# Kernel tuning notes

Hardware: AMD Instinct MI355X
Metric: run time of the kernel (lower is better)

Reference implementation:

```python
import jax, jax.numpy as jnp
import numpy as np

H = 128  # hidden_dim
F = 64   # node_feat_dim


def setup_inputs() -> dict:
    key = jax.random.key(0)
    ks = jax.random.split(key, 24)
    N, E, NR, NT = 50000, 400000, 20000, 20000
    inp = {
        "mol_x": jax.random.normal(ks[0], (N, F), jnp.float32),
        "pos": jax.random.normal(ks[1], (N, 3), jnp.float32),
        "reaction_x": jax.random.normal(ks[2], (NR, F), jnp.float32),
        "target_x": jax.random.normal(ks[3], (NT, F), jnp.float32),
        "edge_index": jax.random.randint(ks[4], (2, E), 0, N, jnp.int32),
    }
    def lin(k, fan_in, fan_out):
        s = 1.0 / np.sqrt(fan_in)
        kw, kb = jax.random.split(k)
        W = jax.random.uniform(kw, (fan_in, fan_out), jnp.float32, -s, s)
        b = jax.random.uniform(kb, (fan_out,), jnp.float32, -s, s)
        return W, b
    inp["W_node"], inp["b_node"] = lin(ks[5], F, H)
    inp["W_att1"], inp["b_att1"] = lin(ks[6], 2 * H + 3, H)
    inp["W_att2"], inp["b_att2"] = lin(ks[7], H, 1)
    inp["W_upd"], inp["b_upd"] = lin(ks[8], H, H)
    inp["Wy1"], inp["by1"] = lin(ks[9], H, 64)
    inp["Wy2"], inp["by2"] = lin(ks[10], 64, 1)
    inp["Wa1"], inp["ba1"] = lin(ks[11], H, 64)
    inp["Wa2"], inp["ba2"] = lin(ks[12], 64, 1)
    return inp


def reference(mol_x, pos, reaction_x, target_x, edge_index,
              W_node, b_node, W_att1, b_att1, W_att2, b_att2,
              W_upd, b_upd, Wy1, by1, Wy2, by2, Wa1, ba1, Wa2, ba2):
    N = mol_x.shape[0]
    # node encoder
    h = mol_x @ W_node + b_node                      # [N, H]
    src, dst = edge_index[0], edge_index[1]          # PyG: x_j = source, x_i = target
    x_j = h[src]                                      # [E, H]
    x_i = h[dst]                                      # [E, H]
    dist = pos[dst] - pos[src]                        # [E, 3]
    cat = jnp.concatenate([x_i, x_j, dist], axis=1)   # [E, 2H+3]
    s = jax.nn.relu(cat @ W_att1 + b_att1) @ W_att2 + b_att2  # [E, 1]
    att = jax.nn.softmax(s, axis=0)                   # global softmax over edges (dim=0)
    msg = x_j * att                                   # [E, H]
    aggr = jax.ops.segment_sum(msg, dst, num_segments=N)  # scatter-add -> [N, H]
    mol_feats = aggr @ W_upd + b_upd                  # [N, H]
    # heads on reaction / target graphs
    rh = reaction_x @ W_node + b_node
    th = target_x @ W_node + b_node
    pred_yield = (jax.nn.relu(rh @ Wy1 + by1) @ Wy2 + by2).squeeze(-1)
    pred_activity = (jax.nn.relu(th @ Wa1 + ba1) @ Wa2 + ba2).squeeze(-1)
    return pred_yield, pred_activity, mol_feats
```

## Files before the change

### kernel.cpp

```cpp
#include <hip/hip_runtime.h>
#include <hip/hip_bf16.h>

typedef unsigned short ushort_t;
typedef __attribute__((ext_vector_type(8))) short s16x8;
typedef __attribute__((ext_vector_type(4))) float f32x4;

__device__ inline unsigned short f2bf(float x) {
    unsigned u = __float_as_uint(x);
    return (unsigned short)((u + 0x7FFFu + ((u >> 16) & 1u)) >> 16);
}
__device__ inline float bflo(unsigned u) { return __uint_as_float(u << 16); }
__device__ inline float bfhi(unsigned u) { return __uint_as_float(u & 0xffff0000u); }

__device__ inline void pack_one(const float* __restrict__ W, int K, int N,
                                ushort_t* __restrict__ dst, int g) {
    int KT = K / 32;
    int nt = g / (KT * 64);
    int rem = g % (KT * 64);
    int kt = rem / 64, lane = rem % 64;
    int n = nt * 16 + (lane & 15);
    int kbase = kt * 32 + ((lane >> 4) << 3);
    ushort_t tmp[8];
#pragma unroll
    for (int j = 0; j < 8; ++j) tmp[j] = f2bf(W[(size_t)(kbase + j) * N + n]);
    uint4 pk;
    pk.x = tmp[0] | ((unsigned)tmp[1] << 16);
    pk.y = tmp[2] | ((unsigned)tmp[3] << 16);
    pk.z = tmp[4] | ((unsigned)tmp[5] << 16);
    pk.w = tmp[6] | ((unsigned)tmp[7] << 16);
    *(uint4*)&dst[(size_t)g * 8] = pk;
}

__global__ void convert_w(const float* __restrict__ Wn, const float* __restrict__ W1,
                          const float* __restrict__ Wu, const float* __restrict__ Wy1,
                          const float* __restrict__ Wa1,
                          ushort_t* __restrict__ Wnb, ushort_t* __restrict__ W1tb,
                          ushort_t* __restrict__ W1mb, ushort_t* __restrict__ Wub,
                          ushort_t* __restrict__ Wy1b, ushort_t* __restrict__ Wa1b,
                          int* __restrict__ counts, int N) {
    int t = blockIdx.x * 256 + threadIdx.x;
    if (t < 1024)       pack_one(Wn, 64, 128, Wnb, t);
    else if (t < 3072)  pack_one(W1, 128, 128, W1tb, t - 1024);
    else if (t < 5120)  pack_one(W1 + 128 * 128, 128, 128, W1mb, t - 3072);
    else if (t < 7168)  pack_one(Wu, 128, 128, Wub, t - 5120);
    else if (t < 8192)  pack_one(Wy1, 128, 64, Wy1b, t - 7168);
    else if (t < 9216)  pack_one(Wa1, 128, 64, Wa1b, t - 8192);
    if (t < N) counts[t] = 0;
}

__global__ void encode_pq(const float* __restrict__ x, const ushort_t* __restrict__ Wnb,
                          const float* __restrict__ bn, const ushort_t* __restrict__ W1tb,
                          const ushort_t* __restrict__ W1mb, const float* __restrict__ b1,
                          ushort_t* __restrict__ hb, ushort_t* __restrict__ P,
                          ushort_t* __restrict__ Q, const int* __restrict__ dst,
                          int* __restrict__ counts, int nrows, int E) {
    __shared__ ushort_t ldsH[4 * 16 * 136];
    int t = threadIdx.x;
    for (int e = blockIdx.x * 256 + t; e < E; e += gridDim.x * 256)
        atomicAdd(&counts[dst[e]], 1);
    int w = t >> 6, lane = t & 63;
    int c = lane & 15, q = lane >> 4;
    int r0 = blockIdx.x * 64 + w * 16;
    int rowA = r0 + c; if (rowA >= nrows) rowA = nrows - 1;
    ushort_t* myH = &ldsH[w * 16 * 136];

    s16x8 xa[2];
#pragma unroll
    for (int kt = 0; kt < 2; ++kt) {
        const float* xp = &x[(size_t)rowA * 64 + kt * 32 + q * 8];
        float4 v0 = *(const float4*)xp;
        float4 v1 = *(const float4*)(xp + 4);
        s16x8 a;
        a[0] = (short)f2bf(v0.x); a[1] = (short)f2bf(v0.y);
        a[2] = (short)f2bf(v0.z); a[3] = (short)f2bf(v0.w);
        a[4] = (short)f2bf(v1.x); a[5] = (short)f2bf(v1.y);
        a[6] = (short)f2bf(v1.z); a[7] = (short)f2bf(v1.w);
        xa[kt] = a;
    }
#pragma unroll
    for (int nt = 0; nt < 8; ++nt) {
        f32x4 acc = {0.f, 0.f, 0.f, 0.f};
#pragma unroll
        for (int kt = 0; kt < 2; ++kt) {
            s16x8 b = *(const s16x8*)&Wnb[((nt * 2 + kt) * 64 + lane) * 8];
            acc = __builtin_amdgcn_mfma_f32_16x16x32_bf16(xa[kt], b, acc, 0, 0, 0);
        }
        float bi = bn[nt * 16 + c];
#pragma unroll
        for (int r = 0; r < 4; ++r) {
            int row = r0 + q * 4 + r;
            ushort_t hv = f2bf(acc[r] + bi);
            myH[(q * 4 + r) * 136 + nt * 16 + c] = hv;
            if (row < nrows) hb[(size_t)row * 128 + nt * 16 + c] = hv;
        }
    }
    __syncthreads();
    s16x8 ha[4];
#pragma unroll
    for (int kt = 0; kt < 4; ++kt)
        ha[kt] = *(const s16x8*)&myH[c * 136 + kt * 32 + q * 8];
#pragma unroll
    for (int nt = 0; nt < 8; ++nt) {
        f32x4 pa = {0.f, 0.f, 0.f, 0.f}, qa = pa;
#pragma unroll
        for (int kt = 0; kt < 4; ++kt) {
            s16x8 bp = *(const s16x8*)&W1tb[((nt * 4 + kt) * 64 + lane) * 8];
            s16x8 bq = *(const s16x8*)&W1mb[((nt * 4 + kt) * 64 + lane) * 8];
            pa = __builtin_amdgcn_mfma_f32_16x16x32_bf16(ha[kt], bp, pa, 0, 0, 0);
            qa = __builtin_amdgcn_mfma_f32_16x16x32_bf16(ha[kt], bq, qa, 0, 0, 0);
        }
        float bi = b1[nt * 16 + c];
#pragma unroll
        for (int r = 0; r < 4; ++r) {
            int row = r0 + q * 4 + r;
            if (row < nrows) {
                P[(size_t)row * 128 + nt * 16 + c] = f2bf(pa[r] + bi);
                Q[(size_t)row * 128 + nt * 16 + c] = f2bf(qa[r]);
            }
        }
    }
}

__global__ void scan1(const int* __restrict__ counts, int* __restrict__ offs,
                      int* __restrict__ partials, int N) {
    __shared__ int sm[256];
    int i = blockIdx.x * 256 + threadIdx.x;
    int v = (i < N) ? counts[i] : 0;
    sm[threadIdx.x] = v; __syncthreads();
    for (int off = 1; off < 256; off <<= 1) {
        int add = (threadIdx.x >= off) ? sm[threadIdx.x - off] : 0;
        __syncthreads();
        sm[threadIdx.x] += add;
        __syncthreads();
    }
    if (i < N) offs[i] = sm[threadIdx.x] - v;
    if (threadIdx.x == 255) partials[blockIdx.x] = sm[255];
}

__global__ void scan_add(int* __restrict__ offs, int* __restrict__ cursor,
                         const int* __restrict__ partials, int nb, int N) {
    __shared__ int sm[256];
    int t = threadIdx.x;
    sm[t] = (t < nb && t < blockIdx.x) ? partials[t] : 0;
    __syncthreads();
    for (int off = 128; off > 0; off >>= 1) {
        if (t < off) sm[t] += sm[t + off];
        __syncthreads();
    }
    int basev = sm[0];
    int i = blockIdx.x * 256 + t;
    if (i < N) {
        int v = offs[i] + basev;
        offs[i] = v;
        cursor[i] = v;
    }
}

__global__ void edge_score(const ushort_t* __restrict__ P, const ushort_t* __restrict__ Q,
                           const float* __restrict__ pos, const int* __restrict__ src,
                           const int* __restrict__ dst, const float* __restrict__ W1b,
                           const float* __restrict__ W2, const float* __restrict__ b2,
                           int* __restrict__ cursor, int2* __restrict__ csr,
                           float* __restrict__ redm, float* __restrict__ rede, int E) {
    __shared__ float wsh[512];
    __shared__ float smm[256], sme[256];
    int t = threadIdx.x;
    for (int i = t; i < 384; i += 256) wsh[i] = W1b[i];
    if (t < 128) wsh[384 + t] = W2[t];
    __syncthreads();
    int w = t >> 6, lane = t & 63;
    int g = lane >> 4, c = lane & 15;
    float w0[8], w1[8], w2[8], wv[8];
#pragma unroll
    for (int j = 0; j < 8; ++j) {
        w0[j] = wsh[c * 8 + j];
        w1[j] = wsh[128 + c * 8 + j];
        w2[j] = wsh[256 + c * 8 + j];
        wv[j] = wsh[384 + c * 8 + j];
    }
    float b2v = b2[0];
    int base = blockIdx.x * 64 + w * 16;
    float m = -1e30f, ev = 0.f;
#pragma unroll
    for (int it = 0; it < 4; ++it) {
        int e = base + it * 4 + g;
        bool valid = e < E;
        int ee = valid ? e : (E - 1);
        int sa = src[ee], da = dst[ee];
        uint4 pr = *(const uint4*)&P[(size_t)da * 128 + c * 8];
        uint4 qr = *(const uint4*)&Q[(size_t)sa * 128 + c * 8];
        float d0 = pos[da * 3]     - pos[sa * 3];
        float d1 = pos[da * 3 + 1] - pos[sa * 3 + 1];
        float d2 = pos[da * 3 + 2] - pos[sa * 3 + 2];
        unsigned pw[4] = {pr.x, pr.y, pr.z, pr.w};
        unsigned qw[4] = {qr.x, qr.y, qr.z, qr.w};
        float v = 0.f;
#pragma unroll
        for (int jj = 0; jj < 4; ++jj) {
            float pe = bflo(pw[jj]) + bflo(qw[jj])
                     + d0 * w0[2 * jj] + d1 * w1[2 * jj] + d2 * w2[2 * jj];
            float po = bfhi(pw[jj]) + bfhi(qw[jj])
                     + d0 * w0[2 * jj + 1] + d1 * w1[2 * jj + 1] + d2 * w2[2 * jj + 1];
            v += fmaxf(pe, 0.f) * wv[2 * jj] + fmaxf(po, 0.f) * wv[2 * jj + 1];
        }
#pragma unroll
        for (int off = 1; off < 16; off <<= 1) v += __shfl_xor(v, off, 64);
        if (c == 0 && valid) {
            float sv = v + b2v;
            int p = atomicAdd(&cursor[da], 1);
            csr[p] = make_int2(sa, __float_as_int(sv));
            float nm = fmaxf(m, sv);
            ev = ev * __expf(m - nm) + __expf(sv - nm);
            m = nm;
        }
    }
    smm[t] = m; sme[t] = ev; __syncthreads();
    for (int off = 128; off > 0; off >>= 1) {
        if (t < off) {
            float m1 = smm[t], m2 = smm[t + off];
            float e1 = sme[t], e2 = sme[t + off];
            float M = fmaxf(m1, m2);
            smm[t] = M;
            sme[t] = e1 * __expf(m1 - M) + e2 * __expf(m2 - M);
        }
        __syncthreads();
    }
    if (t == 0) { redm[blockIdx.x] = smm[0]; rede[blockIdx.x] = sme[0]; }
}

__global__ void smax2(const float* __restrict__ redm, const float* __restrict__ rede,
                      float* __restrict__ scal, int nb) {
    __shared__ float smm[256], sme[256];
    int t = threadIdx.x;
    float m = -1e30f, ev = 0.f;
    for (int i = t; i < nb; i += 256) {
        float m2 = redm[i], e2 = rede[i];
        float M = fmaxf(m, m2);
        ev = ev * __expf(m - M) + e2 * __expf(m2 - M);
        m = M;
    }
    smm[t] = m; sme[t] = ev; __syncthreads();
    for (int off = 128; off > 0; off >>= 1) {
        if (t < off) {
            float m1 = smm[t], m2 = smm[t + off];
            float e1 = sme[t], e2 = sme[t + off];
            float M = fmaxf(m1, m2);
            smm[t] = M;
            sme[t] = e1 * __expf(m1 - M) + e2 * __expf(m2 - M);
        }
        __syncthreads();
    }
    if (t == 0) { scal[0] = smm[0]; scal[1] = 1.f / sme[0]; }
}

__global__ void gather_upd(const ushort_t* __restrict__ hb, const int2* __restrict__ csr,
                           const int* __restrict__ offs, const int* __restrict__ deg,
                           const float* __restrict__ scal,
                           const ushort_t* __restrict__ Wub, const float* __restrict__ bu,
                           float* __restrict__ C, int N) {
    __shared__ ushort_t ldsA[16 * 136];
    int t = threadIdx.x;
    int w = t >> 6, lane = t & 63;
    int g = lane >> 4, c = lane & 15;
    int r0 = blockIdx.x * 16;
    float m = scal[0], inv = scal[1];
#pragma unroll
    for (int i = 0; i < 4; ++i) {
        int node = r0 + w * 4 + i;
        float a[8] = {0.f, 0.f, 0.f, 0.f, 0.f, 0.f, 0.f, 0.f};
        if (node < N) {
            int start = offs[node], d = deg[node];
            for (int k = g; k < d; k += 4) {
                int2 v = csr[start + k];
                float att = __expf(__int_as_float(v.y) - m) * inv;
                uint4 hq = *(const uint4*)&hb[(size_t)v.x * 128 + c * 8];
                a[0] += bflo(hq.x) * att; a[1] += bfhi(hq.x) * att;
                a[2] += bflo(hq.y) * att; a[3] += bfhi(hq.y) * att;
                a[4] += bflo(hq.z) * att; a[5] += bfhi(hq.z) * att;
                a[6] += bflo(hq.w) * att; a[7] += bfhi(hq.w) * att;
            }
        }
#pragma unroll
        for (int j = 0; j < 8; ++j) {
            a[j] += __shfl_xor(a[j], 16, 64);
            a[j] += __shfl_xor(a[j], 32, 64);
        }
        if (g == 0) {
            uint4 pk;
            pk.x = f2bf(a[0]) | ((unsigned)f2bf(a[1]) << 16);
            pk.y = f2bf(a[2]) | ((unsigned)f2bf(a[3]) << 16);
            pk.z = f2bf(a[4]) | ((unsigned)f2bf(a[5]) << 16);
            pk.w = f2bf(a[6]) | ((unsigned)f2bf(a[7]) << 16);
            *(uint4*)&ldsA[(w * 4 + i) * 136 + c * 8] = pk;
        }
    }
    __syncthreads();
    int q = lane >> 4;
    int ntA = w, ntB = w + 4;
    f32x4 acc0 = {0.f, 0.f, 0.f, 0.f}, acc1 = acc0;
#pragma unroll
    for (int kt = 0; kt < 4; ++kt) {
        s16x8 av = *(const s16x8*)&ldsA[c * 136 + kt * 32 + q * 8];
        s16x8 b0 = *(const s16x8*)&Wub[((ntA * 4 + kt) * 64 + lane) * 8];
        s16x8 b1 = *(const s16x8*)&Wub[((ntB * 4 + kt) * 64 + lane) * 8];
        acc0 = __builtin_amdgcn_mfma_f32_16x16x32_bf16(av, b0, acc0, 0, 0, 0);
        acc1 = __builtin_amdgcn_mfma_f32_16x16x32_bf16(av, b1, acc1, 0, 0, 0);
    }
    float bi0 = bu[ntA * 16 + c], bi1 = bu[ntB * 16 + c];
#pragma unroll
    for (int r = 0; r < 4; ++r) {
        int row = r0 + q * 4 + r;
        if (row < N) {
            C[(size_t)row * 128 + ntA * 16 + c] = acc0[r] + bi0;
            C[(size_t)row * 128 + ntB * 16 + c] = acc1[r] + bi1;
        }
    }
}

__global__ void head_mfma(const float* __restrict__ rx, const float* __restrict__ tx,
                          const ushort_t* __restrict__ Wnb, const float* __restrict__ bn,
                          const ushort_t* __restrict__ Wy1b, const float* __restrict__ by1,
                          const float* __restrict__ Wy2, const float* __restrict__ by2,
                          const ushort_t* __restrict__ Wa1b, const float* __restrict__ ba1,
                          const float* __restrict__ Wa2, const float* __restrict__ ba2,
                          float* __restrict__ out, int nb1, int NR, int NT) {
    __shared__ ushort_t ldsA[16 * 72];
    __shared__ ushort_t ldsB[16 * 136];
    __shared__ float part[64];
    int blk = blockIdx.x;
    const float* x; const ushort_t* W1b; const float* b1; const float* W2; const float* b2;
    float* o; int r0, nrows;
    if (blk < nb1) { x = rx; W1b = Wy1b; b1 = by1; W2 = Wy2; b2 = by2; o = out; r0 = blk * 16; nrows = NR; }
    else { x = tx; W1b = Wa1b; b1 = ba1; W2 = Wa2; b2 = ba2; o = out + NR; r0 = (blk - nb1) * 16; nrows = NT; }

    int t = threadIdx.x;
    {
        int row = t >> 4, c4 = (t & 15) * 4;
        float4 v = *(const float4*)&x[(size_t)(r0 + row) * 64 + c4];
        uint2 pk;
        pk.x = f2bf(v.x) | ((unsigned)f2bf(v.y) << 16);
        pk.y = f2bf(v.z) | ((unsigned)f2bf(v.w) << 16);
        *(uint2*)&ldsA[row * 72 + c4] = pk;
    }
    __syncthreads();
    int w = t >> 6, lane = t & 63;
    int c = lane & 15, q = lane >> 4;
    {
        int ntA = w, ntB = w + 4;
        f32x4 acc0 = {0.f, 0.f, 0.f, 0.f}, acc1 = acc0;
#pragma unroll
        for (int kt = 0; kt < 2; ++kt) {
            s16x8 a = *(const s16x8*)&ldsA[c * 72 + kt * 32 + q * 8];
            s16x8 b0 = *(const s16x8*)&Wnb[((ntA * 2 + kt) * 64 + lane) * 8];
            s16x8 b1v = *(const s16x8*)&Wnb[((ntB * 2 + kt) * 64 + lane) * 8];
            acc0 = __builtin_amdgcn_mfma_f32_16x16x32_bf16(a, b0, acc0, 0, 0, 0);
            acc1 = __builtin_amdgcn_mfma_f32_16x16x32_bf16(a, b1v, acc1, 0, 0, 0);
        }
        float bi0 = bn[ntA * 16 + c], bi1 = bn[ntB * 16 + c];
#pragma unroll
        for (int r = 0; r < 4; ++r) {
            int row = q * 4 + r;
            ldsB[row * 136 + ntA * 16 + c] = f2bf(acc0[r] + bi0);
            ldsB[row * 136 + ntB * 16 + c] = f2bf(acc1[r] + bi1);
        }
    }
    __syncthreads();
    {
        f32x4 acc = {0.f, 0.f, 0.f, 0.f};
#pragma unroll
        for (int kt = 0; kt < 4; ++kt) {
            s16x8 a = *(const s16x8*)&ldsB[c * 136 + kt * 32 + q * 8];
            s16x8 b0 = *(const s16x8*)&W1b[((w * 4 + kt) * 64 + lane) * 8];
            acc = __builtin_amdgcn_mfma_f32_16x16x32_bf16(a, b0, acc, 0, 0, 0);
        }
        float bi = b1[w * 16 + c], w2v = W2[w * 16 + c];
#pragma unroll
        for (int r = 0; r < 4; ++r) {
            float u = fmaxf(acc[r] + bi, 0.f) * w2v;
#pragma unroll
            for (int mm = 1; mm < 16; mm <<= 1) u += __shfl_xor(u, mm, 64);
            if (c == 0) part[w * 16 + q * 4 + r] = u;
        }
    }
    __syncthreads();
    if (t < 16) {
        int row = r0 + t;
        if (row < nrows)
            o[row] = part[t] + part[16 + t] + part[32 + t] + part[48 + t] + b2[0];
    }
}

extern "C" void kernel_launch(void* const* d_in, const int* in_sizes, int n_in,
                              void* d_out, int out_size, void* d_ws, size_t ws_size,
                              hipStream_t stream) {
    const float* mol_x      = (const float*)d_in[0];
    const float* pos        = (const float*)d_in[1];
    const float* reaction_x = (const float*)d_in[2];
    const float* target_x   = (const float*)d_in[3];
    const int*   ei         = (const int*)d_in[4];
    const float* W_node = (const float*)d_in[5];
    const float* b_node = (const float*)d_in[6];
    const float* W_att1 = (const float*)d_in[7];
    const float* b_att1 = (const float*)d_in[8];
    const float* W_att2 = (const float*)d_in[9];
    const float* b_att2 = (const float*)d_in[10];
    const float* W_upd  = (const float*)d_in[11];
    const float* b_upd  = (const float*)d_in[12];
    const float* Wy1 = (const float*)d_in[13];
    const float* by1 = (const float*)d_in[14];
    const float* Wy2 = (const float*)d_in[15];
    const float* by2 = (const float*)d_in[16];
    const float* Wa1 = (const float*)d_in[17];
    const float* ba1 = (const float*)d_in[18];
    const float* Wa2 = (const float*)d_in[19];
    const float* ba2 = (const float*)d_in[20];

    int N  = in_sizes[0] / 64;
    int E  = in_sizes[4] / 2;
    int NR = in_sizes[2] / 64;
    int NT = in_sizes[3] / 64;

    float* out = (float*)d_out;

    int nbE = (E + 63) / 64;

    char* wp = (char*)d_ws;
    ushort_t* hb = (ushort_t*)wp;  wp += (size_t)N * 128 * 2;
    ushort_t* Qb = (ushort_t*)wp;  wp += (size_t)N * 128 * 2;
    float* redm  = (float*)wp;     wp += (size_t)nbE * 4;
    float* rede  = (float*)wp;     wp += (size_t)nbE * 4;
    float* scal  = (float*)wp;     wp += 4 * 4;
    int* counts  = (int*)wp;       wp += (size_t)N * 4;
    int* offs    = (int*)wp;       wp += (size_t)N * 4;
    int* cursor  = (int*)wp;       wp += (size_t)N * 4;
    int* partials= (int*)wp;       wp += 256 * 4;
    int2* csr    = (int2*)wp;      wp += (size_t)E * 8;
    ushort_t* Wnb  = (ushort_t*)wp; wp += 8192 * 2;
    ushort_t* W1tb = (ushort_t*)wp; wp += 16384 * 2;
    ushort_t* W1mb = (ushort_t*)wp; wp += 16384 * 2;
    ushort_t* Wub  = (ushort_t*)wp; wp += 16384 * 2;
    ushort_t* Wy1b = (ushort_t*)wp; wp += 8192 * 2;
    ushort_t* Wa1b = (ushort_t*)wp; wp += 8192 * 2;
    ushort_t* Pb = (ushort_t*)(out + NR + NT);
    float* molf  = out + NR + NT;

    const int* srcp = ei;
    const int* dstp = ei + E;
    int nbN = (N + 255) / 256;

    convert_w<<<nbN, 256, 0, stream>>>(W_node, W_att1, W_upd, Wy1, Wa1,
                                       Wnb, W1tb, W1mb, Wub, Wy1b, Wa1b, counts, N);
    encode_pq<<<(N + 63) / 64, 256, 0, stream>>>(mol_x, Wnb, b_node, W1tb, W1mb, b_att1,
                                                 hb, Pb, Qb, dstp, counts, N, E);
    scan1<<<nbN, 256, 0, stream>>>(counts, offs, partials, N);
    scan_add<<<nbN, 256, 0, stream>>>(offs, cursor, partials, nbN, N);
    edge_score<<<nbE, 256, 0, stream>>>(Pb, Qb, pos, srcp, dstp,
                                        W_att1 + 256 * 128, W_att2, b_att2,
                                        cursor, csr, redm, rede, E);
    smax2<<<1, 256, 0, stream>>>(redm, rede, scal, nbE);
    gather_upd<<<(N + 15) / 16, 256, 0, stream>>>(hb, csr, offs, counts, scal,
                                                  Wub, b_upd, molf, N);
    head_mfma<<<(NR + NT) / 16, 256, 0, stream>>>(reaction_x, target_x, Wnb, b_node,
                                                  Wy1b, by1, Wy2, by2, Wa1b, ba1, Wa2, ba2,
                                                  out, NR / 16, NR, NT);
}
```

Measured before the change: 246.9 us.

## Fuse softmax finalize, gather-update and heads into one kernel; widen edge blocks

Removes the single-block smax2 kernel by having every gather block redundantly reduce the per-block max/sum partials, and merges the gather_upd and head_mfma kernels into one launch split by block index. Edge_score now processes 128 edges per block (halving partials) and issues the cursor atomic before the P/Q loads so its latency overlaps. The gather loop is unrolled by two to keep more loads in flight. This cuts two launches and one serial tiny kernel, at the cost of each gather block reading about 3125 partials redundantly.

```diff
diff --git a/kernel.cpp b/kernel.cpp
--- a/kernel.cpp
+++ b/kernel.cpp
@@ -179,14 +179,16 @@
         wv[j] = wsh[384 + c * 8 + j];
     }
     float b2v = b2[0];
-    int base = blockIdx.x * 64 + w * 16;
+    int base = blockIdx.x * 128 + w * 32;
     float m = -1e30f, ev = 0.f;
 #pragma unroll
-    for (int it = 0; it < 4; ++it) {
+    for (int it = 0; it < 8; ++it) {
         int e = base + it * 4 + g;
         bool valid = e < E;
         int ee = valid ? e : (E - 1);
         int sa = src[ee], da = dst[ee];
+        int p = 0;
+        if (c == 0 && valid) p = atomicAdd(&cursor[da], 1);
         uint4 pr = *(const uint4*)&P[(size_t)da * 128 + c * 8];
         uint4 qr = *(const uint4*)&Q[(size_t)sa * 128 + c * 8];
         float d0 = pos[da * 3]     - pos[sa * 3];
@@ -207,7 +209,6 @@
         for (int off = 1; off < 16; off <<= 1) v += __shfl_xor(v, off, 64);
         if (c == 0 && valid) {
             float sv = v + b2v;
-            int p = atomicAdd(&cursor[da], 1);
             csr[p] = make_int2(sa, __float_as_int(sv));
             float nm = fmaxf(m, sv);
             ev = ev * __expf(m - nm) + __expf(sv - nm);
@@ -228,165 +229,177 @@
     if (t == 0) { redm[blockIdx.x] = smm[0]; rede[blockIdx.x] = sme[0]; }
 }
 
-__global__ void smax2(const float* __restrict__ redm, const float* __restrict__ rede,
-                      float* __restrict__ scal, int nb) {
-    __shared__ float smm[256], sme[256];
-    int t = threadIdx.x;
-    float m = -1e30f, ev = 0.f;
-    for (int i = t; i < nb; i += 256) {
-        float m2 = redm[i], e2 = rede[i];
-        float M = fmaxf(m, m2);
-        ev = ev * __expf(m - M) + e2 * __expf(m2 - M);
-        m = M;
-    }
-    smm[t] = m; sme[t] = ev; __syncthreads();
-    for (int off = 128; off > 0; off >>= 1) {
-        if (t < off) {
-            float m1 = smm[t], m2 = smm[t + off];
-            float e1 = sme[t], e2 = sme[t + off];
-            float M = fmaxf(m1, m2);
-            smm[t] = M;
-            sme[t] = e1 * __expf(m1 - M) + e2 * __expf(m2 - M);
-        }
-        __syncthreads();
-    }
-    if (t == 0) { scal[0] = smm[0]; scal[1] = 1.f / sme[0]; }
-}
-
-__global__ void gather_upd(const ushort_t* __restrict__ hb, const int2* __restrict__ csr,
-                           const int* __restrict__ offs, const int* __restrict__ deg,
-                           const float* __restrict__ scal,
-                           const ushort_t* __restrict__ Wub, const float* __restrict__ bu,
-                           float* __restrict__ C, int N) {
-    __shared__ ushort_t ldsA[16 * 136];
+__global__ void gather_head(const ushort_t* __restrict__ hb, const int2* __restrict__ csr,
+                            const int* __restrict__ offs, const int* __restrict__ deg,
+                            const float* __restrict__ redm, const float* __restrict__ rede,
+                            int nbE,
+                            const ushort_t* __restrict__ Wub, const float* __restrict__ bu,
+                            float* __restrict__ molf, int N, int nbG,
+                            const float* __restrict__ rx, const float* __restrict__ tx,
+                            const ushort_t* __restrict__ Wnb, const float* __restrict__ bn,
+                            const ushort_t* __restrict__ Wy1b, const float* __restrict__ by1,
+                            const float* __restrict__ Wy2, const float* __restrict__ by2,
+                            const ushort_t* __restrict__ Wa1b, const float* __restrict__ ba1,
+                            const float* __restrict__ Wa2, const float* __restrict__ ba2,
+                            float* __restrict__ out, int nb1, int NR, int NT) {
     int t = threadIdx.x;
     int w = t >> 6, lane = t & 63;
-    int g = lane >> 4, c = lane & 15;
-    int r0 = blockIdx.x * 16;
-    float m = scal[0], inv = scal[1];
-#pragma unroll
-    for (int i = 0; i < 4; ++i) {
-        int node = r0 + w * 4 + i;
-        float a[8] = {0.f, 0.f, 0.f, 0.f, 0.f, 0.f, 0.f, 0.f};
-        if (node < N) {
-            int start = offs[node], d = deg[node];
-            for (int k = g; k < d; k += 4) {
-                int2 v = csr[start + k];
-                float att = __expf(__int_as_float(v.y) - m) * inv;
-                uint4 hq = *(const uint4*)&hb[(size_t)v.x * 128 + c * 8];
-                a[0] += bflo(hq.x) * att; a[1] += bfhi(hq.x) * att;
-                a[2] += bflo(hq.y) * att; a[3] += bfhi(hq.y) * att;
-                a[4] += bflo(hq.z) * att; a[5] += bfhi(hq.z) * att;
-                a[6] += bflo(hq.w) * att; a[7] += bfhi(hq.w) * att;
-            }
-        }
-#pragma unroll
-        for (int j = 0; j < 8; ++j) {
-            a[j] += __shfl_xor(a[j], 16, 64);
-            a[j] += __shfl_xor(a[j], 32, 64);
-        }
-        if (g == 0) {
-            uint4 pk;
-            pk.x = f2bf(a[0]) | ((unsigned)f2bf(a[1]) << 16);
-            pk.y = f2bf(a[2]) | ((unsigned)f2bf(a[3]) << 16);
-            pk.z = f2bf(a[4]) | ((unsigned)f2bf(a[5]) << 16);
-            pk.w = f2bf(a[6]) | ((unsigned)f2bf(a[7]) << 16);
-            *(uint4*)&ldsA[(w * 4 + i) * 136 + c * 8] = pk;
-        }
-    }
-    __syncthreads();
-    int q = lane >> 4;
-    int ntA = w, ntB = w + 4;
-    f32x4 acc0 = {0.f, 0.f, 0.f, 0.f}, acc1 = acc0;
-#pragma unroll
-    for (int kt = 0; kt < 4; ++kt) {
-        s16x8 av = *(const s16x8*)&ldsA[c * 136 + kt * 32 + q * 8];
-        s16x8 b0 = *(const s16x8*)&Wub[((ntA * 4 + kt) * 64 + lane) * 8];
-        s16x8 b1 = *(const s16x8*)&Wub[((ntB * 4 + kt) * 64 + lane) * 8];
-        acc0 = __builtin_amdgcn_mfma_f32_16x16x32_bf16(av, b0, acc0, 0, 0, 0);
-        acc1 = __builtin_amdgcn_mfma_f32_16x16x32_bf16(av, b1, acc1, 0, 0, 0);
-    }
-    float bi0 = bu[ntA * 16 + c], bi1 = bu[ntB * 16 + c];
-#pragma unroll
-    for (int r = 0; r < 4; ++r) {
-        int row = r0 + q * 4 + r;
-        if (row < N) {
-            C[(size_t)row * 128 + ntA * 16 + c] = acc0[r] + bi0;
-            C[(size_t)row * 128 + ntB * 16 + c] = acc1[r] + bi1;
-        }
-    }
-}
-
-__global__ void head_mfma(const float* __restrict__ rx, const float* __restrict__ tx,
-                          const ushort_t* __restrict__ Wnb, const float* __restrict__ bn,
-                          const ushort_t* __restrict__ Wy1b, const float* __restrict__ by1,
-                          const float* __restrict__ Wy2, const float* __restrict__ by2,
-                          const ushort_t* __restrict__ Wa1b, const float* __restrict__ ba1,
-                          const float* __restrict__ Wa2, const float* __restrict__ ba2,
-                          float* __restrict__ out, int nb1, int NR, int NT) {
-    __shared__ ushort_t ldsA[16 * 72];
-    __shared__ ushort_t ldsB[16 * 136];
-    __shared__ float part[64];
-    int blk = blockIdx.x;
-    const float* x; const ushort_t* W1b; const float* b1; const float* W2; const float* b2;
-    float* o; int r0, nrows;
-    if (blk < nb1) { x = rx; W1b = Wy1b; b1 = by1; W2 = Wy2; b2 = by2; o = out; r0 = blk * 16; nrows = NR; }
-    else { x = tx; W1b = Wa1b; b1 = ba1; W2 = Wa2; b2 = ba2; o = out + NR; r0 = (blk - nb1) * 16; nrows = NT; }
-
-    int t = threadIdx.x;
-    {
-        int row = t >> 4, c4 = (t & 15) * 4;
-        float4 v = *(const float4*)&x[(size_t)(r0 + row) * 64 + c4];
-        uint2 pk;
-        pk.x = f2bf(v.x) | ((unsigned)f2bf(v.y) << 16);
-        pk.y = f2bf(v.z) | ((unsigned)f2bf(v.w) << 16);
-        *(uint2*)&ldsA[row * 72 + c4] = pk;
-    }
-    __syncthreads();
-    int w = t >> 6, lane = t & 63;
     int c = lane & 15, q = lane >> 4;
-    {
+
+    if (blockIdx.x < nbG) {
+        __shared__ ushort_t ldsA[16 * 136];
+        __shared__ float smm[256], sme[256];
+        float m = -1e30f, z = 0.f;
+        for (int i = t; i < nbE; i += 256) {
+            float m2 = redm[i], z2 = rede[i];
+            float M = fmaxf(m, m2);
+            z = z * __expf(m - M) + z2 * __expf(m2 - M);
+            m = M;
+        }
+        smm[t] = m; sme[t] = z; __syncthreads();
+        for (int off = 128; off > 0; off >>= 1) {
+            if (t < off) {
+                float m1 = smm[t], m2 = smm[t + off];
+                float e1 = sme[t], e2 = sme[t + off];
+                float M = fmaxf(m1, m2);
+                smm[t] = M;
+                sme[t] = e1 * __expf(m1 - M) + e2 * __expf(m2 - M);
+            }
+            __syncthreads();
+        }
+        float gm = smm[0], inv = 1.f / sme[0];
+        __syncthreads();
+
+        int g = lane >> 4;
+        int r0 = blockIdx.x * 16;
+#pragma unroll
+        for (int i = 0; i < 4; ++i) {
+            int node = r0 + w * 4 + i;
+            float a[8] = {0.f, 0.f, 0.f, 0.f, 0.f, 0.f, 0.f, 0.f};
+            if (node < N) {
+                int start = offs[node], d = deg[node];
+                int k = g;
+                for (; k + 4 < d; k += 8) {
+                    int2 v0 = csr[start + k];
+                    int2 v1 = csr[start + k + 4];
+                    uint4 h0 = *(const uint4*)&hb[(size_t)v0.x * 128 + c * 8];
+                    uint4 h1 = *(const uint4*)&hb[(size_t)v1.x * 128 + c * 8];
+                    float at0 = __expf(__int_as_float(v0.y) - gm) * inv;
+                    float at1 = __expf(__int_as_float(v1.y) - gm) * inv;
+                    a[0] += bflo(h0.x) * at0; a[1] += bfhi(h0.x) * at0;
+                    a[2] += bflo(h0.y) * at0; a[3] += bfhi(h0.y) * at0;
+                    a[4] += bflo(h0.z) * at0; a[5] += bfhi(h0.z) * at0;
+                    a[6] += bflo(h0.w) * at0; a[7] += bfhi(h0.w) * at0;
+                    a[0] += bflo(h1.x) * at1; a[1] += bfhi(h1.x) * at1;
+                    a[2] += bflo(h1.y) * at1; a[3] += bfhi(h1.y) * at1;
+                    a[4] += bflo(h1.z) * at1; a[5] += bfhi(h1.z) * at1;
+                    a[6] += bflo(h1.w) * at1; a[7] += bfhi(h1.w) * at1;
+                }
+                if (k < d) {
+                    int2 v0 = csr[start + k];
+                    uint4 h0 = *(const uint4*)&hb[(size_t)v0.x * 128 + c * 8];
+                    float at0 = __expf(__int_as_float(v0.y) - gm) * inv;
+                    a[0] += bflo(h0.x) * at0; a[1] += bfhi(h0.x) * at0;
+                    a[2] += bflo(h0.y) * at0; a[3] += bfhi(h0.y) * at0;
+                    a[4] += bflo(h0.z) * at0; a[5] += bfhi(h0.z) * at0;
+                    a[6] += bflo(h0.w) * at0; a[7] += bfhi(h0.w) * at0;
+                }
+            }
+#pragma unroll
+            for (int j = 0; j < 8; ++j) {
+                a[j] += __shfl_xor(a[j], 16, 64);
+                a[j] += __shfl_xor(a[j], 32, 64);
+            }
+            if (g == 0) {
+                uint4 pk;
+                pk.x = f2bf(a[0]) | ((unsigned)f2bf(a[1]) << 16);
+                pk.y = f2bf(a[2]) | ((unsigned)f2bf(a[3]) << 16);
+                pk.z = f2bf(a[4]) | ((unsigned)f2bf(a[5]) << 16);
+                pk.w = f2bf(a[6]) | ((unsigned)f2bf(a[7]) << 16);
+                *(uint4*)&ldsA[(w * 4 + i) * 136 + c * 8] = pk;
+            }
+        }
+        __syncthreads();
         int ntA = w, ntB = w + 4;
         f32x4 acc0 = {0.f, 0.f, 0.f, 0.f}, acc1 = acc0;
 #pragma unroll
-        for (int kt = 0; kt < 2; ++kt) {
-            s16x8 a = *(const s16x8*)&ldsA[c * 72 + kt * 32 + q * 8];
-            s16x8 b0 = *(const s16x8*)&Wnb[((ntA * 2 + kt) * 64 + lane) * 8];
-            s16x8 b1v = *(const s16x8*)&Wnb[((ntB * 2 + kt) * 64 + lane) * 8];
-            acc0 = __builtin_amdgcn_mfma_f32_16x16x32_bf16(a, b0, acc0, 0, 0, 0);
-            acc1 = __builtin_amdgcn_mfma_f32_16x16x32_bf16(a, b1v, acc1, 0, 0, 0);
-        }
-        float bi0 = bn[ntA * 16 + c], bi1 = bn[ntB * 16 + c];
+        for (int kt = 0; kt < 4; ++kt) {
+            s16x8 av = *(const s16x8*)&ldsA[c * 136 + kt * 32 + q * 8];
+            s16x8 b0 = *(const s16x8*)&Wub[((ntA * 4 + kt) * 64 + lane) * 8];
+            s16x8 b1 = *(const s16x8*)&Wub[((ntB * 4 + kt) * 64 + lane) * 8];
+            acc0 = __builtin_amdgcn_mfma_f32_16x16x32_bf16(av, b0, acc0, 0, 0, 0);
+            acc1 = __builtin_amdgcn_mfma_f32_16x16x32_bf16(av, b1, acc1, 0, 0, 0);
+        }
+        float bi0 = bu[ntA * 16 + c], bi1 = bu[ntB * 16 + c];
 #pragma unroll
         for (int r = 0; r < 4; ++r) {
-            int row = q * 4 + r;
-            ldsB[row * 136 + ntA * 16 + c] = f2bf(acc0[r] + bi0);
-            ldsB[row * 136 + ntB * 16 + c] = f2bf(acc1[r] + bi1);
-        }
-    }
-    __syncthreads();
-    {
-        f32x4 acc = {0.f, 0.f, 0.f, 0.f};
-#pragma unroll
-        for (int kt = 0; kt < 4; ++kt) {
-            s16x8 a = *(const s16x8*)&ldsB[c * 136 + kt * 32 + q * 8];
-            s16x8 b0 = *(const s16x8*)&W1b[((w * 4 + kt) * 64 + lane) * 8];
-            acc = __builtin_amdgcn_mfma_f32_16x16x32_bf16(a, b0, acc, 0, 0, 0);
-        }
-        float bi = b1[w * 16 + c], w2v = W2[w * 16 + c];
-#pragma unroll
-        for (int r = 0; r < 4; ++r) {
-            float u = fmaxf(acc[r] + bi, 0.f) * w2v;
-#pragma unroll
-            for (int mm = 1; mm < 16; mm <<= 1) u += __shfl_xor(u, mm, 64);
-            if (c == 0) part[w * 16 + q * 4 + r] = u;
-        }
-    }
-    __syncthreads();
-    if (t < 16) {
-        int row = r0 + t;
-        if (row < nrows)
-            o[row] = part[t] + part[16 + t] + part[32 + t] + part[48 + t] + b2[0];
+            int row = r0 + q * 4 + r;
+            if (row < N) {
+                molf[(size_t)row * 128 + ntA * 16 + c] = acc0[r] + bi0;
+                molf[(size_t)row * 128 + ntB * 16 + c] = acc1[r] + bi1;
+            }
+        }
+    } else {
+        __shared__ ushort_t ldsX[16 * 72];
+        __shared__ ushort_t ldsB[16 * 136];
+        __shared__ float part[64];
+        int blk = blockIdx.x - nbG;
+        const float* x; const ushort_t* W1b; const float* b1; const float* W2; const float* b2;
+        float* o; int r0, nrows;
+        if (blk < nb1) { x = rx; W1b = Wy1b; b1 = by1; W2 = Wy2; b2 = by2; o = out; r0 = blk * 16; nrows = NR; }
+        else { x = tx; W1b = Wa1b; b1 = ba1; W2 = Wa2; b2 = ba2; o = out + NR; r0 = (blk - nb1) * 16; nrows = NT; }
+        {
+            int row = t >> 4, c4 = (t & 15) * 4;
+            float4 v = *(const float4*)&x[(size_t)(r0 + row) * 64 + c4];
+            uint2 pk;
+            pk.x = f2bf(v.x) | ((unsigned)f2bf(v.y) << 16);
+            pk.y = f2bf(v.z) | ((unsigned)f2bf(v.w) << 16);
+            *(uint2*)&ldsX[row * 72 + c4] = pk;
+        }
+        __syncthreads();
+        {
+            int ntA = w, ntB = w + 4;
+            f32x4 acc0 = {0.f, 0.f, 0.f, 0.f}, acc1 = acc0;
+#pragma unroll
+            for (int kt = 0; kt < 2; ++kt) {
+                s16x8 a = *(const s16x8*)&ldsX[c * 72 + kt * 32 + q * 8];
+                s16x8 b0 = *(const s16x8*)&Wnb[((ntA * 2 + kt) * 64 + lane) * 8];
+                s16x8 b1v = *(const s16x8*)&Wnb[((ntB * 2 + kt) * 64 + lane) * 8];
+                acc0 = __builtin_amdgcn_mfma_f32_16x16x32_bf16(a, b0, acc0, 0, 0, 0);
+                acc1 = __builtin_amdgcn_mfma_f32_16x16x32_bf16(a, b1v, acc1, 0, 0, 0);
+            }
+            float bi0 = bn[ntA * 16 + c], bi1 = bn[ntB * 16 + c];
+#pragma unroll
+            for (int r = 0; r < 4; ++r) {
+                int row = q * 4 + r;
+                ldsB[row * 136 + ntA * 16 + c] = f2bf(acc0[r] + bi0);
+                ldsB[row * 136 + ntB * 16 + c] = f2bf(acc1[r] + bi1);
+            }
+        }
+        __syncthreads();
+        {
+            f32x4 acc = {0.f, 0.f, 0.f, 0.f};
+#pragma unroll
+            for (int kt = 0; kt < 4; ++kt) {
+                s16x8 a = *(const s16x8*)&ldsB[c * 136 + kt * 32 + q * 8];
+                s16x8 b0 = *(const s16x8*)&W1b[((w * 4 + kt) * 64 + lane) * 8];
+                acc = __builtin_amdgcn_mfma_f32_16x16x32_bf16(a, b0, acc, 0, 0, 0);
+            }
+            float bi = b1[w * 16 + c], w2v = W2[w * 16 + c];
+#pragma unroll
+            for (int r = 0; r < 4; ++r) {
+                float u = fmaxf(acc[r] + bi, 0.f) * w2v;
+#pragma unroll
+                for (int mm = 1; mm < 16; mm <<= 1) u += __shfl_xor(u, mm, 64);
+                if (c == 0) part[w * 16 + q * 4 + r] = u;
+            }
+        }
+        __syncthreads();
+        if (t < 16) {
+            int row = r0 + t;
+            if (row < nrows)
+                o[row] = part[t] + part[16 + t] + part[32 + t] + part[48 + t] + b2[0];
+        }
     }
 }
 
@@ -422,14 +435,15 @@
 
     float* out = (float*)d_out;
 
-    int nbE = (E + 63) / 64;
+    int nbE = (E + 127) / 128;
+    int nbG = (N + 15) / 16;
+    int nbH = (NR + NT) / 16;
 
     char* wp = (char*)d_ws;
     ushort_t* hb = (ushort_t*)wp;  wp += (size_t)N * 128 * 2;
     ushort_t* Qb = (ushort_t*)wp;  wp += (size_t)N * 128 * 2;
     float* redm  = (float*)wp;     wp += (size_t)nbE * 4;
     float* rede  = (float*)wp;     wp += (size_t)nbE * 4;
-    float* scal  = (float*)wp;     wp += 4 * 4;
     int* counts  = (int*)wp;       wp += (size_t)N * 4;
     int* offs    = (int*)wp;       wp += (size_t)N * 4;
     int* cursor  = (int*)wp;       wp += (size_t)N * 4;
@@ -457,10 +471,9 @@
     edge_score<<<nbE, 256, 0, stream>>>(Pb, Qb, pos, srcp, dstp,
                                         W_att1 + 256 * 128, W_att2, b_att2,
                                         cursor, csr, redm, rede, E);
-    smax2<<<1, 256, 0, stream>>>(redm, rede, scal, nbE);
-    gather_upd<<<(N + 15) / 16, 256, 0, stream>>>(hb, csr, offs, counts, scal,
-                                                  Wub, b_upd, molf, N);
-    head_mfma<<<(NR + NT) / 16, 256, 0, stream>>>(reaction_x, target_x, Wnb, b_node,
-                                                  Wy1b, by1, Wy2, by2, Wa1b, ba1, Wa2, ba2,
-                                                  out, NR / 16, NR, NT);
-}
+    gather_head<<<nbG + nbH, 256, 0, stream>>>(hb, csr, offs, counts, redm, rede, nbE,
+                                               Wub, b_upd, molf, N, nbG,
+                                               reaction_x, target_x, Wnb, b_node,
+                                               Wy1b, by1, Wy2, by2, Wa1b, ba1, Wa2, ba2,
+                                               out, NR / 16, NR, NT);
+}
```

After: 232.3 us. 1.06x faster.
